# Optimization experiments

Measured on AMD Instinct MI355X. Metric: run time of the kernel, lower is better.

## Reference

```python
import jax, jax.numpy as jnp
import numpy as np

BATCH = 32768
HIDDEN = 512
OUT = 2
FUTURE_STEPS = 60


def _lstm_cell(x, h, c, w_ih, w_hh, b_ih, b_hh):
    # PyTorch gate order: i, f, g, o
    g = x @ w_ih.T + h @ w_hh.T + b_ih + b_hh
    i, f, gg, o = jnp.split(g, 4, axis=-1)
    c_new = jax.nn.sigmoid(f) * c + jax.nn.sigmoid(i) * jnp.tanh(gg)
    h_new = jax.nn.sigmoid(o) * jnp.tanh(c_new)
    return h_new, c_new


def setup_inputs() -> dict:
    key = jax.random.key(0)
    ks = jax.random.split(key, 16)
    s = 0.05
    inp = {
        "h": jax.random.normal(ks[0], (BATCH, HIDDEN), jnp.float32),
        "w_init_h": jax.random.normal(ks[1], (HIDDEN, HIDDEN), jnp.float32) * s,
        "b_init_h": jax.random.normal(ks[2], (HIDDEN,), jnp.float32) * s,
        "w_init_c": jax.random.normal(ks[3], (HIDDEN, HIDDEN), jnp.float32) * s,
        "b_init_c": jax.random.normal(ks[4], (HIDDEN,), jnp.float32) * s,
        "w_ih0": jax.random.normal(ks[5], (4 * HIDDEN, OUT), jnp.float32) * s,
        "w_hh0": jax.random.normal(ks[6], (4 * HIDDEN, HIDDEN), jnp.float32) * s,
        "b_ih0": jax.random.normal(ks[7], (4 * HIDDEN,), jnp.float32) * s,
        "b_hh0": jax.random.normal(ks[8], (4 * HIDDEN,), jnp.float32) * s,
        "w_ih1": jax.random.normal(ks[9], (4 * HIDDEN, HIDDEN), jnp.float32) * s,
        "w_hh1": jax.random.normal(ks[10], (4 * HIDDEN, HIDDEN), jnp.float32) * s,
        "b_ih1": jax.random.normal(ks[11], (4 * HIDDEN,), jnp.float32) * s,
        "b_hh1": jax.random.normal(ks[12], (4 * HIDDEN,), jnp.float32) * s,
        "w_out": jax.random.normal(ks[13], (OUT, HIDDEN), jnp.float32) * s,
        "b_out": jax.random.normal(ks[14], (OUT,), jnp.float32) * s,
    }
    return inp


def reference(h, w_init_h, b_init_h, w_init_c, b_init_c,
              w_ih0, w_hh0, b_ih0, b_hh0,
              w_ih1, w_hh1, b_ih1, b_hh1,
              w_out, b_out):
    batch = h.shape[0]
    # same initial (h, c) replicated to both LSTM layers (repeat(2,1,1))
    h0 = h @ w_init_h.T + b_init_h
    c0 = h @ w_init_c.T + b_init_c
    x0 = jnp.zeros((batch, OUT), h.dtype)

    def step(carry, _):
        x, h1, c1, h2, c2 = carry
        h1, c1 = _lstm_cell(x, h1, c1, w_ih0, w_hh0, b_ih0, b_hh0)
        h2, c2 = _lstm_cell(h1, h2, c2, w_ih1, w_hh1, b_ih1, b_hh1)
        pred = h2 @ w_out.T + b_out  # [batch, OUT]
        return (pred, h1, c1, h2, c2), pred

    _, preds = jax.lax.scan(step, (x0, h0, c0, h0, c0), None, length=FUTURE_STEPS)
    return jnp.transpose(preds, (1, 0, 2))  # [batch, future_steps, OUT]
```

## Files before the change

### kernel.cpp

```cpp
#include <hip/hip_runtime.h>

#define HID    512
#define TPB    512
#define NSTEP  60
#define BMI    64

using f32x4 = __attribute__((ext_vector_type(4))) float;
using s16x8 = __attribute__((ext_vector_type(8))) short;

__device__ __forceinline__ unsigned short f2bf(float f) {
    unsigned u = __builtin_bit_cast(unsigned, f);
    u += 0x7fffu + ((u >> 16) & 1u);
    return (unsigned short)(u >> 16);
}
__device__ __forceinline__ float bf2f(unsigned u) {
    return __builtin_bit_cast(float, u << 16);
}
__device__ __forceinline__ float sigm(float x) { return 1.0f / (1.0f + __expf(-x)); }
__device__ __forceinline__ float tanh_(float x) { return 1.0f - 2.0f / (__expf(2.0f * x) + 1.0f); }

__device__ __forceinline__ f32x4 deperm(f32x4 q, int lgr) {
    f32x4 p;
    if (lgr == 0)      { p[0]=q[0]; p[1]=q[1]; p[2]=q[2]; p[3]=q[3]; }
    else if (lgr == 1) { p[0]=q[1]; p[1]=q[0]; p[2]=q[3]; p[3]=q[2]; }
    else if (lgr == 2) { p[0]=q[2]; p[1]=q[3]; p[2]=q[0]; p[3]=q[1]; }
    else               { p[0]=q[3]; p[1]=q[2]; p[2]=q[1]; p[3]=q[0]; }
    return p;
}

__global__ void pack_kernel(const float* __restrict__ w_hh0, const float* __restrict__ w_ih1,
                            const float* __restrict__ w_hh1, const float* __restrict__ w_init_h,
                            const float* __restrict__ w_init_c,
                            const float* __restrict__ b_ih0, const float* __restrict__ b_hh0,
                            const float* __restrict__ b_ih1, const float* __restrict__ b_hh1,
                            unsigned short* __restrict__ PW1, unsigned short* __restrict__ PW2,
                            unsigned short* __restrict__ PI,
                            float* __restrict__ b1, float* __restrict__ b2)
{
    int idx = blockIdx.x * 256 + threadIdx.x;
    if (idx < 1048576) {
        int el = idx & 511, fr = idx >> 9;
        int ks = fr & 15, ct = (fr >> 4) & 7, s = fr >> 7;
        int lane = el >> 3, e = el & 7;
        int cl = ct * 16 + (lane & 15);
        int gcol = (cl >> 5) * 512 + s * 32 + (cl & 31);
        int k = ks * 32 + (lane >> 4) * 8 + e;
        PW1[idx] = f2bf(w_hh0[gcol * 512 + k]);
        return;
    }
    int i2 = idx - 1048576;
    if (i2 >= 0 && i2 < 2097152) {
        int el = i2 & 511, fr = i2 >> 9;
        int ks = fr & 31, ct = (fr >> 5) & 7, s = fr >> 8;
        int lane = el >> 3, e = el & 7;
        int cl = ct * 16 + (lane & 15);
        int gcol = (cl >> 5) * 512 + s * 32 + (cl & 31);
        int kk = (ks & 15) * 32 + (lane >> 4) * 8 + e;
        float v = (ks < 16) ? w_ih1[gcol * 512 + kk] : w_hh1[gcol * 512 + kk];
        PW2[i2] = f2bf(v);
        return;
    }
    int i3 = idx - (1048576 + 2097152);
    if (i3 >= 0 && i3 < 524288) {
        int el = i3 & 511, fr = i3 >> 9;
        int ks = fr & 15, tile = fr >> 4;
        int s = tile >> 5, c = tile & 31;
        int lane = el >> 3, e = el & 7;
        int n = c * 16 + (lane & 15);
        int k = ks * 32 + (lane >> 4) * 8 + e;
        float v = s ? w_init_c[n * 512 + k] : w_init_h[n * 512 + k];
        PI[i3] = f2bf(v);
        return;
    }
    int i4 = idx - (1048576 + 2097152 + 524288);
    if (i4 >= 0 && i4 < 2048) b1[i4] = b_ih0[i4] + b_hh0[i4];
    else if (i4 >= 2048 && i4 < 4096) b2[i4 - 2048] = b_ih1[i4 - 2048] + b_hh1[i4 - 2048];
}

__global__ __launch_bounds__(TPB, 2) void init_kernel(
    const float* __restrict__ hin, const unsigned short* __restrict__ PI,
    const float* __restrict__ b_init_h, const float* __restrict__ b_init_c,
    unsigned short* __restrict__ h1s, unsigned short* __restrict__ h2s,
    unsigned short* __restrict__ c1s, unsigned short* __restrict__ c2s)
{
    __shared__ unsigned short bufA[BMI * HID];
    const int tid = threadIdx.x, lane = tid & 63, wave = tid >> 6;
    const int m0 = blockIdx.x * BMI;
    const int l15 = lane & 15, lg = lane >> 4;
    const int swz = (lane & 7) << 4;

    for (int j = 0; j < 16; ++j) {
        int e = tid * 4 + j * 2048;
        int row = e >> 9, col = e & 511;
        float4 v = *(const float4*)(hin + (size_t)(m0 + row) * HID + col);
        ushort4 w;
        w.x = f2bf(v.x); w.y = f2bf(v.y); w.z = f2bf(v.z); w.w = f2bf(v.w);
        int L = (row * 1024 + col * 2) ^ ((row & 7) << 4);
        *(ushort4*)((char*)bufA + L) = w;
    }
    __syncthreads();

    #pragma unroll 1
    for (int cc = 0; cc < 4; ++cc) {
        int c = wave * 4 + cc;
        int nc = c * 16 + l15;
        f32x4 acc[4][2];
        #pragma unroll
        for (int rt = 0; rt < 4; ++rt)
            #pragma unroll
            for (int s = 0; s < 2; ++s)
                #pragma unroll
                for (int r = 0; r < 4; ++r) acc[rt][s][r] = 0.0f;

        #pragma unroll
        for (int ks = 0; ks < 16; ++ks) {
            s16x8 a[4];
            #pragma unroll
            for (int rt = 0; rt < 4; ++rt) {
                int ao = (rt * 16 + l15) * 1024 + ((ks * 64 + lg * 16) ^ swz);
                a[rt] = *(const s16x8*)((const char*)bufA + ao);
            }
            #pragma unroll
            for (int s = 0; s < 2; ++s) {
                s16x8 b = ((const s16x8*)PI)[((s * 32 + c) * 16 + ks) * 64 + lane];
                #pragma unroll
                for (int rt = 0; rt < 4; ++rt)
                    acc[rt][s] = __builtin_amdgcn_mfma_f32_16x16x32_bf16(a[rt], b, acc[rt][s], 0, 0, 0);
            }
        }
        float bh = b_init_h[nc], bc = b_init_c[nc];
        #pragma unroll
        for (int rt = 0; rt < 4; ++rt)
            #pragma unroll
            for (int r = 0; r < 4; ++r) {
                int m = m0 + rt * 16 + lg * 4 + r;
                float hv = acc[rt][0][r] + bh;
                float cv = acc[rt][1][r] + bc;
                unsigned short hb = f2bf(hv);
                size_t o = (size_t)m * HID + nc;
                h1s[o] = hb; h2s[o] = hb;
                c1s[o] = f2bf(cv); c2s[o] = f2bf(cv);
            }
    }
}

__global__ __launch_bounds__(TPB, 2) void l1_kernel(
    const unsigned short* __restrict__ h1R, unsigned short* __restrict__ h1W,
    unsigned short* __restrict__ c1s, const float* __restrict__ pp,
    float* __restrict__ outp, const unsigned short* __restrict__ PW1,
    const float* __restrict__ b1, const float* __restrict__ w_ih0,
    const float* __restrict__ b_out, int t)
{
    __shared__ __align__(16) unsigned short Ab[16384];
    __shared__ __align__(16) float gl[2][2][2048];
    __shared__ __align__(16) float xls[5120];

    const int tid = threadIdx.x, lane = tid & 63, w = tid >> 6;
    const int b = blockIdx.x;
    const int g = 2 * (b & 7) + (b >> 7);
    const int s = (b >> 3) & 15;
    const int m0 = g * 2048;
    const int l15 = lane & 15, lg = lane >> 4;
    const int cg = w & 1, kh = (w >> 1) & 1, rha = w >> 2;

    s16x8 bw[4][8];
    #pragma unroll
    for (int j = 0; j < 4; ++j)
        #pragma unroll
        for (int ksl = 0; ksl < 8; ++ksl)
            bw[j][ksl] = ((const s16x8*)PW1)[(((s * 8 + cg * 4 + j) * 16) + kh * 8 + ksl) * 64 + lane];

    const int erow = tid >> 4, ejp = tid & 15;
    const int lgr = w & 3;
    float b1v[8], wiA[8], wiB[8];
    #pragma unroll
    for (int q = 0; q < 8; ++q) {
        int dj = q & 1, gq = q >> 1;
        int gcol = gq * 512 + s * 32 + ejp * 2 + dj;
        b1v[q] = b1[gcol];
        wiA[q] = w_ih0[gcol * 2 + 0];
        wiB[q] = w_ih0[gcol * 2 + 1];
    }
    float bo0 = b_out[0], bo1 = b_out[1];

    if (t == 0) {
        #pragma unroll
        for (int i = 0; i < 8; ++i) xls[tid * 8 + i] = 0.0f;
    } else {
        f32x4 s0 = {0.f,0.f,0.f,0.f}, s1 = {0.f,0.f,0.f,0.f};
        #pragma unroll 1
        for (int ss = 0; ss < 16; ++ss) {
            const float* p = pp + (((size_t)(g * 16 + ss)) << 12) + tid * 8;
            s0 += *(const f32x4*)p;
            s1 += *(const f32x4*)(p + 4);
        }
        s0[0] += bo0; s0[1] += bo1; s0[2] += bo0; s0[3] += bo1;
        s1[0] += bo0; s1[1] += bo1; s1[2] += bo0; s1[3] += bo1;
        *(f32x4*)(xls + tid * 8) = s0;
        *(f32x4*)(xls + tid * 8 + 4) = s1;
        if (s == 0) {
            float* ob = outp + (size_t)(m0 + tid * 4) * (2 * NSTEP) + (t - 1) * 2;
            *(float2*)(ob)                 = make_float2(s0[0], s0[1]);
            *(float2*)(ob + 2 * NSTEP)     = make_float2(s0[2], s0[3]);
            *(float2*)(ob + 4 * NSTEP)     = make_float2(s1[0], s1[1]);
            *(float2*)(ob + 6 * NSTEP)     = make_float2(s1[2], s1[3]);
        }
    }

    const int st_l15 = tid & 15, st_lg = (tid >> 4) & 3, st_rh = (tid >> 6) & 1, st_kq = tid >> 7;
    const int st_grow = st_rh * 16 + st_l15;

    uint4 nv[4];
    #pragma unroll
    for (int p = 0; p < 4; ++p) {
        int ks = p * 4 + st_kq;
        nv[p] = *(const uint4*)(h1R + (size_t)(m0 + st_grow) * HID + ks * 32 + st_lg * 8);
    }
    #pragma unroll
    for (int p = 0; p < 4; ++p)
        *(uint4*)((char*)Ab + p * 8192 + tid * 16) = nv[p];

    #pragma unroll 1
    for (int ch = 0; ch < 64; ++ch) {
        __syncthreads();

        if (ch < 63) {
            #pragma unroll
            for (int p = 0; p < 4; ++p) {
                int ks = p * 4 + st_kq;
                nv[p] = *(const uint4*)(h1R + (size_t)(m0 + (ch + 1) * 32 + st_grow) * HID + ks * 32 + st_lg * 8);
            }
        }

        f32x4 acc[4];
        #pragma unroll
        for (int j = 0; j < 4; ++j) { acc[j][0]=0.f; acc[j][1]=0.f; acc[j][2]=0.f; acc[j][3]=0.f; }
        #pragma unroll
        for (int ksl = 0; ksl < 8; ++ksl) {
            int ks = kh * 8 + ksl;
            s16x8 a = *(const s16x8*)((const char*)Ab + ks * 2048 + rha * 1024 + lane * 16);
            #pragma unroll
            for (int j = 0; j < 4; ++j)
                acc[j] = __builtin_amdgcn_mfma_f32_16x16x32_bf16(a, bw[j][ksl], acc[j], 0, 0, 0);
        }
        #pragma unroll
        for (int j = 0; j < 4; ++j) {
            int col = (cg * 4 + j) * 16 + l15;
            int u = col & 31, gate = col >> 5;
            float* dst = &gl[kh][u & 1][(u >> 1) * 4 + (gate ^ lg)];
            #pragma unroll
            for (int r = 0; r < 4; ++r)
                dst[(rha * 16 + lg * 4 + r) * 64] = acc[j][r];
        }
        __syncthreads();

        if (ch < 63) {
            #pragma unroll
            for (int p = 0; p < 4; ++p)
                *(uint4*)((char*)Ab + p * 8192 + tid * 16) = nv[p];
        }

        {
            int grow = ch * 32 + erow;
            int m = m0 + grow;
            float x0 = xls[grow * 2 + 0], x1 = xls[grow * 2 + 1];
            int gbase = erow * 64 + ejp * 4;
            f32x4 qa = *(const f32x4*)&gl[0][0][gbase];
            qa += *(const f32x4*)&gl[1][0][gbase];
            f32x4 qb = *(const f32x4*)&gl[0][1][gbase];
            qb += *(const f32x4*)&gl[1][1][gbase];
            qa = deperm(qa, lgr); qb = deperm(qb, lgr);

            int cix = m * HID + s * 32 + ejp * 2;
            unsigned cp = *(const unsigned*)(c1s + cix);
            float cold0 = bf2f(cp & 0xffffu), cold1 = bf2f(cp >> 16);
            float i0 = sigm(qa[0] + b1v[0] + x0 * wiA[0] + x1 * wiB[0]);
            float f0 = sigm(qa[1] + b1v[2] + x0 * wiA[2] + x1 * wiB[2]);
            float g0 = tanh_(qa[2] + b1v[4] + x0 * wiA[4] + x1 * wiB[4]);
            float o0 = sigm(qa[3] + b1v[6] + x0 * wiA[6] + x1 * wiB[6]);
            float cn0 = f0 * cold0 + i0 * g0;
            float hn0 = o0 * tanh_(cn0);
            float i1 = sigm(qb[0] + b1v[1] + x0 * wiA[1] + x1 * wiB[1]);
            float f1 = sigm(qb[1] + b1v[3] + x0 * wiA[3] + x1 * wiB[3]);
            float g1 = tanh_(qb[2] + b1v[5] + x0 * wiA[5] + x1 * wiB[5]);
            float o1 = sigm(qb[3] + b1v[7] + x0 * wiA[7] + x1 * wiB[7]);
            float cn1 = f1 * cold1 + i1 * g1;
            float hn1 = o1 * tanh_(cn1);
            __builtin_nontemporal_store((unsigned)f2bf(cn0) | ((unsigned)f2bf(cn1) << 16),
                                        (unsigned*)(c1s + cix));
            __builtin_nontemporal_store((unsigned)f2bf(hn0) | ((unsigned)f2bf(hn1) << 16),
                                        (unsigned*)(h1W + cix));
        }
    }
}

__global__ __launch_bounds__(TPB, 2) void l2_kernel(
    const unsigned short* __restrict__ h1C, const unsigned short* __restrict__ h2R,
    unsigned short* __restrict__ h2W, unsigned short* __restrict__ c2s,
    float* __restrict__ pp,
    const unsigned short* __restrict__ PW2, const float* __restrict__ b2,
    const float* __restrict__ w_out)
{
    __shared__ __align__(16) unsigned short Ab[32768];
    __shared__ __align__(16) float gl[2][2][2304];

    const int tid = threadIdx.x, lane = tid & 63, w = tid >> 6;
    const int b = blockIdx.x;
    const int g = 2 * (b & 7) + (b >> 7);
    const int s = (b >> 3) & 15;
    const int m0 = g * 2048;
    const int l15 = lane & 15, lg = lane >> 4;
    const int cg = w & 1, kq = w >> 1;
    const int copy = kq >> 1, adder = ((kq & 1) == 0);

    s16x8 bw[4][8];
    #pragma unroll
    for (int j = 0; j < 4; ++j)
        #pragma unroll
        for (int ksl = 0; ksl < 8; ++ksl)
            bw[j][ksl] = ((const s16x8*)PW2)[(((s * 8 + cg * 4 + j) * 32) + kq * 8 + ksl) * 64 + lane];

    const int erow = tid >> 4, ejp = tid & 15;
    const int lgr = w & 3;
    float b2v[8];
    #pragma unroll
    for (int q = 0; q < 8; ++q) {
        int dj = q & 1, gq = q >> 1;
        b2v[q] = b2[gq * 512 + s * 32 + ejp * 2 + dj];
    }
    float woA0 = w_out[s * 32 + ejp * 2], woA1 = w_out[s * 32 + ejp * 2 + 1];
    float woB0 = w_out[512 + s * 32 + ejp * 2], woB1 = w_out[512 + s * 32 + ejp * 2 + 1];

    const int st_l15 = tid & 15, st_lg = (tid >> 4) & 3, st_rh = (tid >> 6) & 1, st_kq = tid >> 7;
    const int st_grow = st_rh * 16 + st_l15;

    uint4 nv[8];
    #pragma unroll
    for (int p = 0; p < 8; ++p) {
        int ks = p * 4 + st_kq;
        const unsigned short* src = (ks < 16) ? h1C : h2R;
        int kel = (ks < 16) ? ks : (ks - 16);
        nv[p] = *(const uint4*)(src + (size_t)(m0 + st_grow) * HID + kel * 32 + st_lg * 8);
    }
    #pragma unroll
    for (int p = 0; p < 8; ++p)
        *(uint4*)((char*)Ab + p * 8192 + tid * 16) = nv[p];

    #pragma unroll 1
    for (int ch = 0; ch < 64; ++ch) {
        __syncthreads();

        if (ch < 63) {
            #pragma unroll
            for (int p = 0; p < 8; ++p) {
                int ks = p * 4 + st_kq;
                const unsigned short* src = (ks < 16) ? h1C : h2R;
                int kel = (ks < 16) ? ks : (ks - 16);
                nv[p] = *(const uint4*)(src + (size_t)(m0 + (ch + 1) * 32 + st_grow) * HID + kel * 32 + st_lg * 8);
            }
        }

        f32x4 acc[2][4];
        #pragma unroll
        for (int rh = 0; rh < 2; ++rh)
            #pragma unroll
            for (int j = 0; j < 4; ++j) { acc[rh][j][0]=0.f; acc[rh][j][1]=0.f; acc[rh][j][2]=0.f; acc[rh][j][3]=0.f; }
        #pragma unroll
        for (int ksl = 0; ksl < 8; ++ksl) {
            int ks = kq * 8 + ksl;
            s16x8 a0 = *(const s16x8*)((const char*)Ab + ks * 2048 + lane * 16);
            s16x8 a1 = *(const s16x8*)((const char*)Ab + ks * 2048 + 1024 + lane * 16);
            #pragma unroll
            for (int j = 0; j < 4; ++j) {
                acc[0][j] = __builtin_amdgcn_mfma_f32_16x16x32_bf16(a0, bw[j][ksl], acc[0][j], 0, 0, 0);
                acc[1][j] = __builtin_amdgcn_mfma_f32_16x16x32_bf16(a1, bw[j][ksl], acc[1][j], 0, 0, 0);
            }
        }

        if (!adder) {
            #pragma unroll
            for (int j = 0; j < 4; ++j) {
                int col = (cg * 4 + j) * 16 + l15;
                int u = col & 31, gate = col >> 5;
                float* dst = &gl[copy][u & 1][(u >> 1) * 4 + (gate ^ lg)];
                #pragma unroll
                for (int rh = 0; rh < 2; ++rh)
                    #pragma unroll
                    for (int r = 0; r < 4; ++r)
                        dst[(rh * 16 + lg * 4 + r) * 64] = acc[rh][j][r];
            }
        }
        __syncthreads();
        if (adder) {
            #pragma unroll
            for (int j = 0; j < 4; ++j) {
                int col = (cg * 4 + j) * 16 + l15;
                int u = col & 31, gate = col >> 5;
                float* dst = &gl[copy][u & 1][(u >> 1) * 4 + (gate ^ lg)];
                #pragma unroll
                for (int rh = 0; rh < 2; ++rh)
                    #pragma unroll
                    for (int r = 0; r < 4; ++r)
                        dst[(rh * 16 + lg * 4 + r) * 64] += acc[rh][j][r];
            }
        }
        __syncthreads();

        if (ch < 63) {
            #pragma unroll
            for (int p = 0; p < 8; ++p)
                *(uint4*)((char*)Ab + p * 8192 + tid * 16) = nv[p];
        }

        {
            int m = m0 + ch * 32 + erow;
            int gbase = erow * 64 + ejp * 4;
            f32x4 qa = *(const f32x4*)&gl[0][0][gbase];
            qa += *(const f32x4*)&gl[1][0][gbase];
            f32x4 qb = *(const f32x4*)&gl[0][1][gbase];
            qb += *(const f32x4*)&gl[1][1][gbase];
            qa = deperm(qa, lgr); qb = deperm(qb, lgr);

            int cix = m * HID + s * 32 + ejp * 2;
            unsigned cp = *(const unsigned*)(c2s + cix);
            float cold0 = bf2f(cp & 0xffffu), cold1 = bf2f(cp >> 16);
            float i0 = sigm(qa[0] + b2v[0]);
            float f0 = sigm(qa[1] + b2v[2]);
            float g0 = tanh_(qa[2] + b2v[4]);
            float o0 = sigm(qa[3] + b2v[6]);
            float cn0 = f0 * cold0 + i0 * g0;
            float hn0 = o0 * tanh_(cn0);
            float i1 = sigm(qb[0] + b2v[1]);
            float f1 = sigm(qb[1] + b2v[3]);
            float g1 = tanh_(qb[2] + b2v[5]);
            float o1 = sigm(qb[3] + b2v[7]);
            float cn1 = f1 * cold1 + i1 * g1;
            float hn1 = o1 * tanh_(cn1);
            __builtin_nontemporal_store((unsigned)f2bf(cn0) | ((unsigned)f2bf(cn1) << 16),
                                        (unsigned*)(c2s + cix));
            __builtin_nontemporal_store((unsigned)f2bf(hn0) | ((unsigned)f2bf(hn1) << 16),
                                        (unsigned*)(h2W + cix));

            float p0 = hn0 * woA0 + hn1 * woA1;
            float p1 = hn0 * woB0 + hn1 * woB1;
            #pragma unroll
            for (int d = 1; d < 16; d <<= 1) {
                p0 += __shfl_xor(p0, d, 16);
                p1 += __shfl_xor(p1, d, 16);
            }
            if (ejp == 0)
                *(float2*)(pp + (((size_t)(g * 16 + s)) << 12) + (size_t)(ch * 32 + erow) * 2)
                    = make_float2(p0, p1);
        }
    }
}

__global__ void tail_kernel(const float* __restrict__ pp, const float* __restrict__ b_out,
                            float* __restrict__ outp)
{
    int i = blockIdx.x * 256 + threadIdx.x;
    if (i < 65536) {
        int m = i >> 1, j = i & 1;
        int g = m >> 11;
        int idx = (m & 2047) * 2 + j;
        float sum = b_out[j];
        #pragma unroll 1
        for (int s = 0; s < 16; ++s)
            sum += pp[(((size_t)(g * 16 + s)) << 12) + idx];
        outp[(size_t)m * (2 * NSTEP) + (NSTEP - 1) * 2 + j] = sum;
    }
}

extern "C" void kernel_launch(void* const* d_in, const int* in_sizes, int n_in,
                              void* d_out, int out_size, void* d_ws, size_t ws_size,
                              hipStream_t stream)
{
    (void)in_sizes; (void)n_in; (void)out_size; (void)ws_size;
    const float* h        = (const float*)d_in[0];
    const float* w_init_h = (const float*)d_in[1];
    const float* b_init_h = (const float*)d_in[2];
    const float* w_init_c = (const float*)d_in[3];
    const float* b_init_c = (const float*)d_in[4];
    const float* w_ih0    = (const float*)d_in[5];
    const float* w_hh0    = (const float*)d_in[6];
    const float* b_ih0    = (const float*)d_in[7];
    const float* b_hh0    = (const float*)d_in[8];
    const float* w_ih1    = (const float*)d_in[9];
    const float* w_hh1    = (const float*)d_in[10];
    const float* b_ih1    = (const float*)d_in[11];
    const float* b_hh1    = (const float*)d_in[12];
    const float* w_out    = (const float*)d_in[13];
    const float* b_out    = (const float*)d_in[14];
    float* out = (float*)d_out;

    char* ws = (char*)d_ws;
    unsigned short* h1s[2] = { (unsigned short*)(ws + 0),
                               (unsigned short*)(ws + 33554432) };
    unsigned short* h2s[2] = { (unsigned short*)(ws + 67108864),
                               (unsigned short*)(ws + 100663296) };
    unsigned short* c1s = (unsigned short*)(ws + 134217728);
    unsigned short* c2s = (unsigned short*)(ws + 167772160);
    float* pp           = (float*)(ws + 201326592);
    unsigned short* PW1 = (unsigned short*)(ws + 205520896);
    unsigned short* PW2 = (unsigned short*)(ws + 207618048);
    unsigned short* PI  = (unsigned short*)(ws + 211812352);
    float* b1 = (float*)(ws + 212860928);
    float* b2 = (float*)(ws + 212869120);

    pack_kernel<<<14352, 256, 0, stream>>>(w_hh0, w_ih1, w_hh1, w_init_h, w_init_c,
                                           b_ih0, b_hh0, b_ih1, b_hh1, PW1, PW2, PI, b1, b2);
    init_kernel<<<32768 / BMI, TPB, 0, stream>>>(h, PI, b_init_h, b_init_c,
                                                 h1s[1], h2s[1], c1s, c2s);
    for (int t = 0; t < NSTEP; ++t) {
        const unsigned short* h1R = h1s[(t + 1) & 1];
        unsigned short* h1W = h1s[t & 1];
        const unsigned short* h2R = h2s[(t + 1) & 1];
        unsigned short* h2W = h2s[t & 1];
        l1_kernel<<<256, TPB, 0, stream>>>(h1R, h1W, c1s, pp, out, PW1, b1, w_ih0, b_out, t);
        l2_kernel<<<256, TPB, 0, stream>>>(h1W, h2R, h2W, c2s, pp, PW2, b2, w_out);
    }
    tail_kernel<<<256, 256, 0, stream>>>(pp, b_out, out);
}
```

Baseline: 41.11 ms.

## Give each wave full-K column tiles and double-buffer A tiles

Repacks the weights so each MFMA column tile holds all four gates of four hidden units. Each wave now owns one column tile over the full K range, so the cross-wave split-K reduction through shared memory and two of the three barriers per chunk are gone. The gate epilogue runs directly from a per-wave scratch transpose. The A tile in LDS is double-buffered, with global prefetch two chunks ahead and the old cell state prefetched as well, leaving one barrier per chunk. In exchange, the doubled LDS footprint and larger per-wave weight register arrays (16 or 32 s16x8) may reduce occupancy under launch_bounds(512,2). Cell and hidden stores also become scalar 16-bit writes instead of packed nontemporal 32-bit ones.

```diff
diff --git a/kernel.cpp b/kernel.cpp
--- a/kernel.cpp
+++ b/kernel.cpp
@@ -18,15 +18,6 @@
 }
 __device__ __forceinline__ float sigm(float x) { return 1.0f / (1.0f + __expf(-x)); }
 __device__ __forceinline__ float tanh_(float x) { return 1.0f - 2.0f / (__expf(2.0f * x) + 1.0f); }
-
-__device__ __forceinline__ f32x4 deperm(f32x4 q, int lgr) {
-    f32x4 p;
-    if (lgr == 0)      { p[0]=q[0]; p[1]=q[1]; p[2]=q[2]; p[3]=q[3]; }
-    else if (lgr == 1) { p[0]=q[1]; p[1]=q[0]; p[2]=q[3]; p[3]=q[2]; }
-    else if (lgr == 2) { p[0]=q[2]; p[1]=q[3]; p[2]=q[0]; p[3]=q[1]; }
-    else               { p[0]=q[3]; p[1]=q[2]; p[2]=q[1]; p[3]=q[0]; }
-    return p;
-}
 
 __global__ void pack_kernel(const float* __restrict__ w_hh0, const float* __restrict__ w_ih1,
                             const float* __restrict__ w_hh1, const float* __restrict__ w_init_h,
@@ -42,8 +33,8 @@
         int el = idx & 511, fr = idx >> 9;
         int ks = fr & 15, ct = (fr >> 4) & 7, s = fr >> 7;
         int lane = el >> 3, e = el & 7;
-        int cl = ct * 16 + (lane & 15);
-        int gcol = (cl >> 5) * 512 + s * 32 + (cl & 31);
+        int l15 = lane & 15;
+        int gcol = (l15 & 3) * 512 + s * 32 + ct * 4 + (l15 >> 2);
         int k = ks * 32 + (lane >> 4) * 8 + e;
         PW1[idx] = f2bf(w_hh0[gcol * 512 + k]);
         return;
@@ -53,8 +44,8 @@
         int el = i2 & 511, fr = i2 >> 9;
         int ks = fr & 31, ct = (fr >> 5) & 7, s = fr >> 8;
         int lane = el >> 3, e = el & 7;
-        int cl = ct * 16 + (lane & 15);
-        int gcol = (cl >> 5) * 512 + s * 32 + (cl & 31);
+        int l15 = lane & 15;
+        int gcol = (l15 & 3) * 512 + s * 32 + ct * 4 + (l15 >> 2);
         int kk = (ks & 15) * 32 + (lane >> 4) * 8 + e;
         float v = (ks < 16) ? w_ih1[gcol * 512 + kk] : w_hh1[gcol * 512 + kk];
         PW2[i2] = f2bf(v);
@@ -151,9 +142,9 @@
     const float* __restrict__ b1, const float* __restrict__ w_ih0,
     const float* __restrict__ b_out, int t)
 {
-    __shared__ __align__(16) unsigned short Ab[16384];
-    __shared__ __align__(16) float gl[2][2][2048];
-    __shared__ __align__(16) float xls[5120];
+    __shared__ __align__(16) unsigned short Ab[2 * 16384];
+    __shared__ __align__(16) float xls[4096];
+    __shared__ __align__(16) float tsc[8 * 320];
 
     const int tid = threadIdx.x, lane = tid & 63, w = tid >> 6;
     const int b = blockIdx.x;
@@ -161,25 +152,23 @@
     const int s = (b >> 3) & 15;
     const int m0 = g * 2048;
     const int l15 = lane & 15, lg = lane >> 4;
-    const int cg = w & 1, kh = (w >> 1) & 1, rha = w >> 2;
-
-    s16x8 bw[4][8];
-    #pragma unroll
-    for (int j = 0; j < 4; ++j)
-        #pragma unroll
-        for (int ksl = 0; ksl < 8; ++ksl)
-            bw[j][ksl] = ((const s16x8*)PW1)[(((s * 8 + cg * 4 + j) * 16) + kh * 8 + ksl) * 64 + lane];
-
-    const int erow = tid >> 4, ejp = tid & 15;
-    const int lgr = w & 3;
-    float b1v[8], wiA[8], wiB[8];
-    #pragma unroll
-    for (int q = 0; q < 8; ++q) {
-        int dj = q & 1, gq = q >> 1;
-        int gcol = gq * 512 + s * 32 + ejp * 2 + dj;
-        b1v[q] = b1[gcol];
-        wiA[q] = w_ih0[gcol * 2 + 0];
-        wiB[q] = w_ih0[gcol * 2 + 1];
+    const int q = l15 & 3, a = l15 >> 2;
+    const int ct = w;
+    const int hid = s * 32 + ct * 4 + a;
+    float* const ts = tsc + w * 320;
+
+    s16x8 bw[16];
+    #pragma unroll
+    for (int ks = 0; ks < 16; ++ks)
+        bw[ks] = ((const s16x8*)PW1)[((s * 8 + ct) * 16 + ks) * 64 + lane];
+
+    float b1v[4], wiA[4], wiB[4];
+    #pragma unroll
+    for (int k = 0; k < 4; ++k) {
+        int gc = k * 512 + hid;
+        b1v[k] = b1[gc];
+        wiA[k] = w_ih0[gc * 2 + 0];
+        wiB[k] = w_ih0[gc * 2 + 1];
     }
     float bo0 = b_out[0], bo1 = b_out[1];
 
@@ -200,10 +189,10 @@
         *(f32x4*)(xls + tid * 8 + 4) = s1;
         if (s == 0) {
             float* ob = outp + (size_t)(m0 + tid * 4) * (2 * NSTEP) + (t - 1) * 2;
-            *(float2*)(ob)                 = make_float2(s0[0], s0[1]);
-            *(float2*)(ob + 2 * NSTEP)     = make_float2(s0[2], s0[3]);
-            *(float2*)(ob + 4 * NSTEP)     = make_float2(s1[0], s1[1]);
-            *(float2*)(ob + 6 * NSTEP)     = make_float2(s1[2], s1[3]);
+            *(float2*)(ob)             = make_float2(s0[0], s0[1]);
+            *(float2*)(ob + 2 * NSTEP) = make_float2(s0[2], s0[3]);
+            *(float2*)(ob + 4 * NSTEP) = make_float2(s1[0], s1[1]);
+            *(float2*)(ob + 6 * NSTEP) = make_float2(s1[2], s1[3]);
         }
     }
 
@@ -214,83 +203,81 @@
     #pragma unroll
     for (int p = 0; p < 4; ++p) {
         int ks = p * 4 + st_kq;
-        nv[p] = *(const uint4*)(h1R + (size_t)(m0 + st_grow) * HID + ks * 32 + st_lg * 8);
-    }
-    #pragma unroll
-    for (int p = 0; p < 4; ++p)
-        *(uint4*)((char*)Ab + p * 8192 + tid * 16) = nv[p];
+        uint4 v = *(const uint4*)(h1R + (size_t)(m0 + st_grow) * HID + ks * 32 + st_lg * 8);
+        *(uint4*)((char*)Ab + p * 8192 + tid * 16) = v;
+    }
+    #pragma unroll
+    for (int p = 0; p < 4; ++p) {
+        int ks = p * 4 + st_kq;
+        nv[p] = *(const uint4*)(h1R + (size_t)(m0 + 32 + st_grow) * HID + ks * 32 + st_lg * 8);
+    }
+    unsigned short cpr0 = c1s[(size_t)(m0 + lg * 4 + q) * HID + hid];
+    unsigned short cpr1 = c1s[(size_t)(m0 + 16 + lg * 4 + q) * HID + hid];
+    __syncthreads();
 
     #pragma unroll 1
     for (int ch = 0; ch < 64; ++ch) {
-        __syncthreads();
-
         if (ch < 63) {
+            char* AbW = (char*)Ab + ((ch + 1) & 1) * 32768;
+            #pragma unroll
+            for (int p = 0; p < 4; ++p)
+                *(uint4*)(AbW + p * 8192 + tid * 16) = nv[p];
+        }
+        if (ch < 62) {
             #pragma unroll
             for (int p = 0; p < 4; ++p) {
                 int ks = p * 4 + st_kq;
-                nv[p] = *(const uint4*)(h1R + (size_t)(m0 + (ch + 1) * 32 + st_grow) * HID + ks * 32 + st_lg * 8);
-            }
-        }
-
-        f32x4 acc[4];
-        #pragma unroll
-        for (int j = 0; j < 4; ++j) { acc[j][0]=0.f; acc[j][1]=0.f; acc[j][2]=0.f; acc[j][3]=0.f; }
+                nv[p] = *(const uint4*)(h1R + (size_t)(m0 + (ch + 2) * 32 + st_grow) * HID + ks * 32 + st_lg * 8);
+            }
+        }
+        unsigned short cnx0 = 0, cnx1 = 0;
+        if (ch < 63) {
+            cnx0 = c1s[(size_t)(m0 + (ch + 1) * 32 + lg * 4 + q) * HID + hid];
+            cnx1 = c1s[(size_t)(m0 + (ch + 1) * 32 + 16 + lg * 4 + q) * HID + hid];
+        }
+
+        const char* AbR = (const char*)Ab + (ch & 1) * 32768;
+        f32x4 a0A = {0.f,0.f,0.f,0.f}, a0B = {0.f,0.f,0.f,0.f};
+        f32x4 a1A = {0.f,0.f,0.f,0.f}, a1B = {0.f,0.f,0.f,0.f};
         #pragma unroll
         for (int ksl = 0; ksl < 8; ++ksl) {
-            int ks = kh * 8 + ksl;
-            s16x8 a = *(const s16x8*)((const char*)Ab + ks * 2048 + rha * 1024 + lane * 16);
-            #pragma unroll
-            for (int j = 0; j < 4; ++j)
-                acc[j] = __builtin_amdgcn_mfma_f32_16x16x32_bf16(a, bw[j][ksl], acc[j], 0, 0, 0);
-        }
-        #pragma unroll
-        for (int j = 0; j < 4; ++j) {
-            int col = (cg * 4 + j) * 16 + l15;
-            int u = col & 31, gate = col >> 5;
-            float* dst = &gl[kh][u & 1][(u >> 1) * 4 + (gate ^ lg)];
+            s16x8 x0 = *(const s16x8*)(AbR + ksl * 2048 + lane * 16);
+            s16x8 x1 = *(const s16x8*)(AbR + ksl * 2048 + 1024 + lane * 16);
+            a0A = __builtin_amdgcn_mfma_f32_16x16x32_bf16(x0, bw[ksl], a0A, 0, 0, 0);
+            a1A = __builtin_amdgcn_mfma_f32_16x16x32_bf16(x1, bw[ksl], a1A, 0, 0, 0);
+        }
+        #pragma unroll
+        for (int ksl = 8; ksl < 16; ++ksl) {
+            s16x8 x0 = *(const s16x8*)(AbR + ksl * 2048 + lane * 16);
+            s16x8 x1 = *(const s16x8*)(AbR + ksl * 2048 + 1024 + lane * 16);
+            a0B = __builtin_amdgcn_mfma_f32_16x16x32_bf16(x0, bw[ksl], a0B, 0, 0, 0);
+            a1B = __builtin_amdgcn_mfma_f32_16x16x32_bf16(x1, bw[ksl], a1B, 0, 0, 0);
+        }
+        f32x4 acS0 = a0A + a0B, acS1 = a1A + a1B;
+
+        #pragma unroll
+        for (int rh = 0; rh < 2; ++rh) {
+            f32x4 ac = rh ? acS1 : acS0;
             #pragma unroll
             for (int r = 0; r < 4; ++r)
-                dst[(rha * 16 + lg * 4 + r) * 64] = acc[j][r];
-        }
+                ts[(lg * 4 + r) * 20 + l15] = ac[r];
+            f32x4 gq = *(const f32x4*)(ts + (lg * 4 + q) * 20 + a * 4);
+
+            int grow = ch * 32 + rh * 16 + lg * 4 + q;
+            float2 xv = *(const float2*)(xls + grow * 2);
+            float iv = sigm(gq[0] + b1v[0] + xv.x * wiA[0] + xv.y * wiB[0]);
+            float fv = sigm(gq[1] + b1v[1] + xv.x * wiA[1] + xv.y * wiB[1]);
+            float gv = tanh_(gq[2] + b1v[2] + xv.x * wiA[2] + xv.y * wiB[2]);
+            float ov = sigm(gq[3] + b1v[3] + xv.x * wiA[3] + xv.y * wiB[3]);
+            float cold = bf2f(rh ? cpr1 : cpr0);
+            float cn = fv * cold + iv * gv;
+            float hn = ov * tanh_(cn);
+            size_t cix = (size_t)(m0 + grow) * HID + hid;
+            c1s[cix] = f2bf(cn);
+            h1W[cix] = f2bf(hn);
+        }
+        cpr0 = cnx0; cpr1 = cnx1;
         __syncthreads();
-
-        if (ch < 63) {
-            #pragma unroll
-            for (int p = 0; p < 4; ++p)
-                *(uint4*)((char*)Ab + p * 8192 + tid * 16) = nv[p];
-        }
-
-        {
-            int grow = ch * 32 + erow;
-            int m = m0 + grow;
-            float x0 = xls[grow * 2 + 0], x1 = xls[grow * 2 + 1];
-            int gbase = erow * 64 + ejp * 4;
-            f32x4 qa = *(const f32x4*)&gl[0][0][gbase];
-            qa += *(const f32x4*)&gl[1][0][gbase];
-            f32x4 qb = *(const f32x4*)&gl[0][1][gbase];
-            qb += *(const f32x4*)&gl[1][1][gbase];
-            qa = deperm(qa, lgr); qb = deperm(qb, lgr);
-
-            int cix = m * HID + s * 32 + ejp * 2;
-            unsigned cp = *(const unsigned*)(c1s + cix);
-            float cold0 = bf2f(cp & 0xffffu), cold1 = bf2f(cp >> 16);
-            float i0 = sigm(qa[0] + b1v[0] + x0 * wiA[0] + x1 * wiB[0]);
-            float f0 = sigm(qa[1] + b1v[2] + x0 * wiA[2] + x1 * wiB[2]);
-            float g0 = tanh_(qa[2] + b1v[4] + x0 * wiA[4] + x1 * wiB[4]);
-            float o0 = sigm(qa[3] + b1v[6] + x0 * wiA[6] + x1 * wiB[6]);
-            float cn0 = f0 * cold0 + i0 * g0;
-            float hn0 = o0 * tanh_(cn0);
-            float i1 = sigm(qb[0] + b1v[1] + x0 * wiA[1] + x1 * wiB[1]);
-            float f1 = sigm(qb[1] + b1v[3] + x0 * wiA[3] + x1 * wiB[3]);
-            float g1 = tanh_(qb[2] + b1v[5] + x0 * wiA[5] + x1 * wiB[5]);
-            float o1 = sigm(qb[3] + b1v[7] + x0 * wiA[7] + x1 * wiB[7]);
-            float cn1 = f1 * cold1 + i1 * g1;
-            float hn1 = o1 * tanh_(cn1);
-            __builtin_nontemporal_store((unsigned)f2bf(cn0) | ((unsigned)f2bf(cn1) << 16),
-                                        (unsigned*)(c1s + cix));
-            __builtin_nontemporal_store((unsigned)f2bf(hn0) | ((unsigned)f2bf(hn1) << 16),
-                                        (unsigned*)(h1W + cix));
-        }
     }
 }
 
@@ -301,8 +288,9 @@
     const unsigned short* __restrict__ PW2, const float* __restrict__ b2,
     const float* __restrict__ w_out)
 {
-    __shared__ __align__(16) unsigned short Ab[32768];
-    __shared__ __align__(16) float gl[2][2][2304];
+    __shared__ __align__(16) unsigned short Ab[2 * 32768];
+    __shared__ __align__(16) float pl[2][32][2][9];
+    __shared__ __align__(16) float tsc[8 * 320];
 
     const int tid = threadIdx.x, lane = tid & 63, w = tid >> 6;
     const int b = blockIdx.x;
@@ -310,26 +298,20 @@
     const int s = (b >> 3) & 15;
     const int m0 = g * 2048;
     const int l15 = lane & 15, lg = lane >> 4;
-    const int cg = w & 1, kq = w >> 1;
-    const int copy = kq >> 1, adder = ((kq & 1) == 0);
-
-    s16x8 bw[4][8];
-    #pragma unroll
-    for (int j = 0; j < 4; ++j)
-        #pragma unroll
-        for (int ksl = 0; ksl < 8; ++ksl)
-            bw[j][ksl] = ((const s16x8*)PW2)[(((s * 8 + cg * 4 + j) * 32) + kq * 8 + ksl) * 64 + lane];
-
-    const int erow = tid >> 4, ejp = tid & 15;
-    const int lgr = w & 3;
-    float b2v[8];
-    #pragma unroll
-    for (int q = 0; q < 8; ++q) {
-        int dj = q & 1, gq = q >> 1;
-        b2v[q] = b2[gq * 512 + s * 32 + ejp * 2 + dj];
-    }
-    float woA0 = w_out[s * 32 + ejp * 2], woA1 = w_out[s * 32 + ejp * 2 + 1];
-    float woB0 = w_out[512 + s * 32 + ejp * 2], woB1 = w_out[512 + s * 32 + ejp * 2 + 1];
+    const int q = l15 & 3, a = l15 >> 2;
+    const int ct = w;
+    const int hid = s * 32 + ct * 4 + a;
+    float* const ts = tsc + w * 320;
+
+    s16x8 bw[32];
+    #pragma unroll
+    for (int ks = 0; ks < 32; ++ks)
+        bw[ks] = ((const s16x8*)PW2)[((s * 8 + ct) * 32 + ks) * 64 + lane];
+
+    float b2v[4];
+    #pragma unroll
+    for (int k = 0; k < 4; ++k) b2v[k] = b2[k * 512 + hid];
+    const float wo0 = w_out[hid], wo1 = w_out[512 + hid];
 
     const int st_l15 = tid & 15, st_lg = (tid >> 4) & 3, st_rh = (tid >> 6) & 1, st_kq = tid >> 7;
     const int st_grow = st_rh * 16 + st_l15;
@@ -340,118 +322,104 @@
         int ks = p * 4 + st_kq;
         const unsigned short* src = (ks < 16) ? h1C : h2R;
         int kel = (ks < 16) ? ks : (ks - 16);
-        nv[p] = *(const uint4*)(src + (size_t)(m0 + st_grow) * HID + kel * 32 + st_lg * 8);
-    }
-    #pragma unroll
-    for (int p = 0; p < 8; ++p)
-        *(uint4*)((char*)Ab + p * 8192 + tid * 16) = nv[p];
+        uint4 v = *(const uint4*)(src + (size_t)(m0 + st_grow) * HID + kel * 32 + st_lg * 8);
+        *(uint4*)((char*)Ab + p * 8192 + tid * 16) = v;
+    }
+    #pragma unroll
+    for (int p = 0; p < 8; ++p) {
+        int ks = p * 4 + st_kq;
+        const unsigned short* src = (ks < 16) ? h1C : h2R;
+        int kel = (ks < 16) ? ks : (ks - 16);
+        nv[p] = *(const uint4*)(src + (size_t)(m0 + 32 + st_grow) * HID + kel * 32 + st_lg * 8);
+    }
+    unsigned short cpr0 = c2s[(size_t)(m0 + lg * 4 + q) * HID + hid];
+    unsigned short cpr1 = c2s[(size_t)(m0 + 16 + lg * 4 + q) * HID + hid];
+    __syncthreads();
 
     #pragma unroll 1
     for (int ch = 0; ch < 64; ++ch) {
-        __syncthreads();
-
         if (ch < 63) {
+            char* AbW = (char*)Ab + ((ch + 1) & 1) * 65536;
+            #pragma unroll
+            for (int p = 0; p < 8; ++p)
+                *(uint4*)(AbW + p * 8192 + tid * 16) = nv[p];
+        }
+        if (ch < 62) {
             #pragma unroll
             for (int p = 0; p < 8; ++p) {
                 int ks = p * 4 + st_kq;
                 const unsigned short* src = (ks < 16) ? h1C : h2R;
                 int kel = (ks < 16) ? ks : (ks - 16);
-                nv[p] = *(const uint4*)(src + (size_t)(m0 + (ch + 1) * 32 + st_grow) * HID + kel * 32 + st_lg * 8);
-            }
-        }
-
-        f32x4 acc[2][4];
-        #pragma unroll
-        for (int rh = 0; rh < 2; ++rh)
-            #pragma unroll
-            for (int j = 0; j < 4; ++j) { acc[rh][j][0]=0.f; acc[rh][j][1]=0.f; acc[rh][j][2]=0.f; acc[rh][j][3]=0.f; }
-        #pragma unroll
-        for (int ksl = 0; ksl < 8; ++ksl) {
-            int ks = kq * 8 + ksl;
-            s16x8 a0 = *(const s16x8*)((const char*)Ab + ks * 2048 + lane * 16);
-            s16x8 a1 = *(const s16x8*)((const char*)Ab + ks * 2048 + 1024 + lane * 16);
-            #pragma unroll
-            for (int j = 0; j < 4; ++j) {
-                acc[0][j] = __builtin_amdgcn_mfma_f32_16x16x32_bf16(a0, bw[j][ksl], acc[0][j], 0, 0, 0);
-                acc[1][j] = __builtin_amdgcn_mfma_f32_16x16x32_bf16(a1, bw[j][ksl], acc[1][j], 0, 0, 0);
-            }
-        }
-
-        if (!adder) {
-            #pragma unroll
-            for (int j = 0; j < 4; ++j) {
-                int col = (cg * 4 + j) * 16 + l15;
-                int u = col & 31, gate = col >> 5;
-                float* dst = &gl[copy][u & 1][(u >> 1) * 4 + (gate ^ lg)];
-                #pragma unroll
-                for (int rh = 0; rh < 2; ++rh)
-                    #pragma unroll
-                    for (int r = 0; r < 4; ++r)
-                        dst[(rh * 16 + lg * 4 + r) * 64] = acc[rh][j][r];
-            }
-        }
+                nv[p] = *(const uint4*)(src + (size_t)(m0 + (ch + 2) * 32 + st_grow) * HID + kel * 32 + st_lg * 8);
+            }
+        }
+        unsigned short cnx0 = 0, cnx1 = 0;
+        if (ch < 63) {
+            cnx0 = c2s[(size_t)(m0 + (ch + 1) * 32 + lg * 4 + q) * HID + hid];
+            cnx1 = c2s[(size_t)(m0 + (ch + 1) * 32 + 16 + lg * 4 + q) * HID + hid];
+        }
+
+        const char* AbR = (const char*)Ab + (ch & 1) * 65536;
+        f32x4 a0A = {0.f,0.f,0.f,0.f}, a0B = {0.f,0.f,0.f,0.f};
+        f32x4 a1A = {0.f,0.f,0.f,0.f}, a1B = {0.f,0.f,0.f,0.f};
+        #pragma unroll
+        for (int ksl = 0; ksl < 16; ++ksl) {
+            s16x8 x0 = *(const s16x8*)(AbR + ksl * 2048 + lane * 16);
+            s16x8 x1 = *(const s16x8*)(AbR + ksl * 2048 + 1024 + lane * 16);
+            a0A = __builtin_amdgcn_mfma_f32_16x16x32_bf16(x0, bw[ksl], a0A, 0, 0, 0);
+            a1A = __builtin_amdgcn_mfma_f32_16x16x32_bf16(x1, bw[ksl], a1A, 0, 0, 0);
+        }
+        #pragma unroll
+        for (int ksl = 16; ksl < 32; ++ksl) {
+            s16x8 x0 = *(const s16x8*)(AbR + ksl * 2048 + lane * 16);
+            s16x8 x1 = *(const s16x8*)(AbR + ksl * 2048 + 1024 + lane * 16);
+            a0B = __builtin_amdgcn_mfma_f32_16x16x32_bf16(x0, bw[ksl], a0B, 0, 0, 0);
+            a1B = __builtin_amdgcn_mfma_f32_16x16x32_bf16(x1, bw[ksl], a1B, 0, 0, 0);
+        }
+        f32x4 acS0 = a0A + a0B, acS1 = a1A + a1B;
+
+        #pragma unroll
+        for (int rh = 0; rh < 2; ++rh) {
+            f32x4 ac = rh ? acS1 : acS0;
+            #pragma unroll
+            for (int r = 0; r < 4; ++r)
+                ts[(lg * 4 + r) * 20 + l15] = ac[r];
+            f32x4 gq = *(const f32x4*)(ts + (lg * 4 + q) * 20 + a * 4);
+
+            int rloc = rh * 16 + lg * 4 + q;
+            int grow = ch * 32 + rloc;
+            float iv = sigm(gq[0] + b2v[0]);
+            float fv = sigm(gq[1] + b2v[1]);
+            float gv = tanh_(gq[2] + b2v[2]);
+            float ov = sigm(gq[3] + b2v[3]);
+            float cold = bf2f(rh ? cpr1 : cpr0);
+            float cn = fv * cold + iv * gv;
+            float hn = ov * tanh_(cn);
+            size_t cix = (size_t)(m0 + grow) * HID + hid;
+            c2s[cix] = f2bf(cn);
+            h2W[cix] = f2bf(hn);
+            float p0 = hn * wo0, p1 = hn * wo1;
+            p0 += __shfl_xor(p0, 4); p0 += __shfl_xor(p0, 8);
+            p1 += __shfl_xor(p1, 4); p1 += __shfl_xor(p1, 8);
+            if (a == 0) {
+                pl[ch & 1][rloc][0][ct] = p0;
+                pl[ch & 1][rloc][1][ct] = p1;
+            }
+        }
+        if (ch > 0 && tid < 64) {
+            int row = tid >> 1, j = tid & 1;
+            const float* pr = &pl[(ch - 1) & 1][row][j][0];
+            float sum = pr[0] + pr[1] + pr[2] + pr[3] + pr[4] + pr[5] + pr[6] + pr[7];
+            pp[((size_t)(g * 16 + s)) * 4096 + (size_t)((ch - 1) * 32 + row) * 2 + j] = sum;
+        }
+        cpr0 = cnx0; cpr1 = cnx1;
         __syncthreads();
-        if (adder) {
-            #pragma unroll
-            for (int j = 0; j < 4; ++j) {
-                int col = (cg * 4 + j) * 16 + l15;
-                int u = col & 31, gate = col >> 5;
-                float* dst = &gl[copy][u & 1][(u >> 1) * 4 + (gate ^ lg)];
-                #pragma unroll
-                for (int rh = 0; rh < 2; ++rh)
-                    #pragma unroll
-                    for (int r = 0; r < 4; ++r)
-                        dst[(rh * 16 + lg * 4 + r) * 64] += acc[rh][j][r];
-            }
-        }
-        __syncthreads();
-
-        if (ch < 63) {
-            #pragma unroll
-            for (int p = 0; p < 8; ++p)
-                *(uint4*)((char*)Ab + p * 8192 + tid * 16) = nv[p];
-        }
-
-        {
-            int m = m0 + ch * 32 + erow;
-            int gbase = erow * 64 + ejp * 4;
-            f32x4 qa = *(const f32x4*)&gl[0][0][gbase];
-            qa += *(const f32x4*)&gl[1][0][gbase];
-            f32x4 qb = *(const f32x4*)&gl[0][1][gbase];
-            qb += *(const f32x4*)&gl[1][1][gbase];
-            qa = deperm(qa, lgr); qb = deperm(qb, lgr);
-
-            int cix = m * HID + s * 32 + ejp * 2;
-            unsigned cp = *(const unsigned*)(c2s + cix);
-            float cold0 = bf2f(cp & 0xffffu), cold1 = bf2f(cp >> 16);
-            float i0 = sigm(qa[0] + b2v[0]);
-            float f0 = sigm(qa[1] + b2v[2]);
-            float g0 = tanh_(qa[2] + b2v[4]);
-            float o0 = sigm(qa[3] + b2v[6]);
-            float cn0 = f0 * cold0 + i0 * g0;
-            float hn0 = o0 * tanh_(cn0);
-            float i1 = sigm(qb[0] + b2v[1]);
-            float f1 = sigm(qb[1] + b2v[3]);
-            float g1 = tanh_(qb[2] + b2v[5]);
-            float o1 = sigm(qb[3] + b2v[7]);
-            float cn1 = f1 * cold1 + i1 * g1;
-            float hn1 = o1 * tanh_(cn1);
-            __builtin_nontemporal_store((unsigned)f2bf(cn0) | ((unsigned)f2bf(cn1) << 16),
-                                        (unsigned*)(c2s + cix));
-            __builtin_nontemporal_store((unsigned)f2bf(hn0) | ((unsigned)f2bf(hn1) << 16),
-                                        (unsigned*)(h2W + cix));
-
-            float p0 = hn0 * woA0 + hn1 * woA1;
-            float p1 = hn0 * woB0 + hn1 * woB1;
-            #pragma unroll
-            for (int d = 1; d < 16; d <<= 1) {
-                p0 += __shfl_xor(p0, d, 16);
-                p1 += __shfl_xor(p1, d, 16);
-            }
-            if (ejp == 0)
-                *(float2*)(pp + (((size_t)(g * 16 + s)) << 12) + (size_t)(ch * 32 + erow) * 2)
-                    = make_float2(p0, p1);
-        }
+    }
+    if (tid < 64) {
+        int row = tid >> 1, j = tid & 1;
+        const float* pr = &pl[1][row][j][0];
+        float sum = pr[0] + pr[1] + pr[2] + pr[3] + pr[4] + pr[5] + pr[6] + pr[7];
+        pp[((size_t)(g * 16 + s)) * 4096 + (size_t)(63 * 32 + row) * 2 + j] = sum;
     }
 }
 
```

Result: faster. 38.21 ms (-7.1%).
